# Performance work log

Hardware: AMD Instinct MI355X
Metric: run time of the kernel (lower is better)

Reference implementation:

```python
import jax, jax.numpy as jnp
import numpy as np


def setup_inputs() -> dict:
    key = jax.random.key(0)
    k1, k2, k3, k4, k5 = jax.random.split(key, 5)
    B, N, M, D = 4096, 2048, 2048, 9
    return {
        "x": jax.random.normal(k1, (B, N), dtype=jnp.float32),
        "eternal_weights": jax.random.normal(k2, (D, N, M), dtype=jnp.float32),
        "eternal_biases": jax.random.normal(k3, (M,), dtype=jnp.float32),
        "classical_weights": jax.random.normal(k4, (N, M), dtype=jnp.float32),
        "classical_biases": jax.random.normal(k5, (M,), dtype=jnp.float32),
    }


def _eternal_probs(eternal_weights, n, m):
    # The gate matrix is cos*I - sin*P + sin*P^T with P the circular shift,
    # so (gate @ s)[i] = cos*s[i] - sin*s[(i+1)%n] + sin*s[(i-1)%n].
    # Vectorize over all m output units at once: state is [m, n].
    state0 = jnp.full((m, n), 1.0 / np.sqrt(n), dtype=eternal_weights.dtype)
    angles = eternal_weights[:, :m, :3]  # [D, m, 3] -- weights[depth, j, 0/1/2]

    def gate(state, angle):  # angle: [m]
        c = jnp.cos(angle)[:, None]
        s = jnp.sin(angle)[:, None]
        return c * state - s * jnp.roll(state, -1, axis=1) + s * jnp.roll(state, 1, axis=1)

    def step(state, ang):  # ang: [m, 3] -- consciousness, intelligence, wisdom
        state = gate(state, ang[:, 0])
        state = gate(state, ang[:, 1])
        state = gate(state, ang[:, 2])
        return state, None

    state, _ = jax.lax.scan(step, state0, angles)
    return jnp.abs(state[:, 0]) ** 2  # [m]


def reference(x, eternal_weights, eternal_biases, classical_weights, classical_biases):
    # eternal_biases exists as a parameter in the original module but is unused in forward.
    n = x.shape[1]
    m = classical_weights.shape[1]
    classical = x @ classical_weights + classical_biases  # [B, m]
    probs = _eternal_probs(eternal_weights, n, m)  # [m], identical for every batch row
    return jnp.tanh(classical + probs[None, :])
```

## Files before the change

kernel.cpp:

```cpp
#include <hip/hip_runtime.h>
#include <hip/hip_fp8.h>
#include <stdint.h>

static constexpr int MM = 4096;
static constexpr int KK = 2048;
static constexpr int NN = 2048;

typedef float floatx16 __attribute__((ext_vector_type(16)));
typedef __bf16 bf16x8 __attribute__((ext_vector_type(8)));
typedef unsigned short u16x8 __attribute__((ext_vector_type(8)));
typedef int intx4 __attribute__((ext_vector_type(4)));
typedef int intx8 __attribute__((ext_vector_type(8)));
typedef unsigned char u8x16 __attribute__((ext_vector_type(16)));

__device__ __forceinline__ unsigned short bf16_rne(float x) {
  union { float f; uint32_t u; } c; c.f = x;
  uint32_t u = c.u;
  u += 0x7fffu + ((u >> 16) & 1u);
  return (unsigned short)(u >> 16);
}
__device__ __forceinline__ float bf16_as_f32(unsigned short h) {
  union { float f; uint32_t u; } c; c.u = ((uint32_t)h) << 16;
  return c.f;
}
__device__ __forceinline__ unsigned char f32_to_e4m3(float x) {
  __hip_fp8_e4m3 q(x);
  return (unsigned char)q.__x;
}
__device__ __forceinline__ float fast_tanh(float x) {
  float e = __expf(2.0f * x);
  return 1.0f - 2.0f / (e + 1.0f);
}


__global__ __launch_bounds__(256) void split_x_kernel(
    const float* __restrict__ in, unsigned short* __restrict__ ahi,
    unsigned char* __restrict__ a8, unsigned char* __restrict__ al8,
    int nunits) {
  int idx = blockIdx.x * 256 + threadIdx.x;
  if (idx >= nunits) return;
  int row = idx >> 7;
  int u = idx & 127;
  int g = u >> 2;
  int c4 = u & 3;
  const float4* s = (const float4*)(in + (size_t)row * KK + u * 16);
  float v[16];
#pragma unroll
  for (int q = 0; q < 4; q++) {
    float4 t = s[q];
    v[q * 4 + 0] = t.x; v[q * 4 + 1] = t.y; v[q * 4 + 2] = t.z; v[q * 4 + 3] = t.w;
  }
  unsigned short h[16];
  u8x16 f8, fl8;
#pragma unroll
  for (int e = 0; e < 16; e++) {
    h[e] = bf16_rne(v[e]);
    float lo = v[e] - bf16_as_f32(h[e]);
    f8[e] = f32_to_e4m3(v[e]);
    fl8[e] = f32_to_e4m3(lo * 512.0f);
  }
  size_t rb = (size_t)row * KK;
#pragma unroll
  for (int cc = 0; cc < 2; cc++) {
    int c8 = c4 * 2 + cc;
    int phys8 = (c8 + row + (row >> 3)) & 7;
    u16x8 o;
#pragma unroll
    for (int e = 0; e < 8; e++) o[e] = h[cc * 8 + e];
    *(u16x8*)(ahi + rb + g * 64 + phys8 * 8) = o;
  }
  int phys4 = (c4 + (row >> 1) + (row >> 3)) & 3;
  *(u8x16*)(a8 + rb + g * 64 + phys4 * 16) = f8;
  *(u8x16*)(al8 + rb + g * 64 + phys4 * 16) = fl8;
}

__global__ __launch_bounds__(256) void wsplit_kernel(
    const float* __restrict__ W, unsigned short* __restrict__ bhi,
    unsigned char* __restrict__ b8, unsigned char* __restrict__ bl8) {
  __shared__ float tile[64][65];
  const int tid = threadIdx.x;
  const int n0 = blockIdx.x * 64;
  const int k0 = blockIdx.y * 64;
#pragma unroll
  for (int i = 0; i < 4; i++) {
    int t = tid + i * 256;
    int kr = t >> 4;
    int nc = (t & 15) * 4;
    const float4 v = *(const float4*)(W + (size_t)(k0 + kr) * NN + n0 + nc);
    tile[nc + 0][kr] = v.x;
    tile[nc + 1][kr] = v.y;
    tile[nc + 2][kr] = v.z;
    tile[nc + 3][kr] = v.w;
  }
  __syncthreads();
  const int nl = tid >> 2;
  const int q = tid & 3;
  const int n = n0 + nl;
  float v[16];
  unsigned short h[16];
  u8x16 f8, fl8;
#pragma unroll
  for (int e = 0; e < 16; e++) {
    v[e] = tile[nl][q * 16 + e];
    h[e] = bf16_rne(v[e]);
    float lo = v[e] - bf16_as_f32(h[e]);
    f8[e] = f32_to_e4m3(v[e]);
    fl8[e] = f32_to_e4m3(lo * 512.0f);
  }
  size_t rb = (size_t)n * KK + k0;
#pragma unroll
  for (int cc = 0; cc < 2; cc++) {
    int c8 = q * 2 + cc;
    int phys8 = (c8 + n + (n >> 3)) & 7;
    u16x8 o;
#pragma unroll
    for (int e = 0; e < 8; e++) o[e] = h[cc * 8 + e];
    *(u16x8*)(bhi + rb + phys8 * 8) = o;
  }
  int phys4 = (q + (n >> 1) + (n >> 3)) & 3;
  *(u8x16*)(b8 + rb + phys4 * 16) = f8;
  *(u8x16*)(bl8 + rb + phys4 * 16) = fl8;
}

__global__ __launch_bounds__(64) void bias_probs_kernel(
    const float* __restrict__ E, const float* __restrict__ cb,
    float* __restrict__ bias2) {
  int i = blockIdx.x * 64 + threadIdx.x;
  if (i >= NN) return;
  float p = 1.0f / 2048.0f;
#pragma unroll
  for (int d = 0; d < 9; d++) {
    const float4 a = *(const float4*)(E + (size_t)d * (2048 * 2048) + (size_t)i * 2048);
    float c0 = cosf(a.x), c1 = cosf(a.y), c2 = cosf(a.z);
    p *= (c0 * c0) * (c1 * c1) * (c2 * c2);
  }
  bias2[i] = cb[i] + p;
}

#define GLL(dst, src)                                                        \
  __builtin_amdgcn_global_load_lds(                                          \
      (const __attribute__((address_space(1))) void*)(src),                  \
      (__attribute__((address_space(3))) void*)(dst), 16, 0, 0)

__global__ __launch_bounds__(256, 2) void gemm_tanh_kernel(
    const unsigned short* __restrict__ Ahi, const unsigned char* __restrict__ A8,
    const unsigned char* __restrict__ Al8,
    const unsigned short* __restrict__ Bhi, const unsigned char* __restrict__ B8,
    const unsigned char* __restrict__ Bl8,
    const float* __restrict__ bias2, float* __restrict__ out) {
  __shared__ __align__(16) unsigned short sAh[128 * 64];
  __shared__ __align__(16) unsigned short sBh[128 * 64];
  __shared__ __align__(16) unsigned char sA8[128 * 64];
  __shared__ __align__(16) unsigned char sAl[128 * 64];
  __shared__ __align__(16) unsigned char sB8[128 * 64];
  __shared__ __align__(16) unsigned char sBl[128 * 64];

  const int tid = threadIdx.x;
  const int lane = tid & 63;
  const int wave = tid >> 6;
  const int wm = (wave >> 1) * 64;
  const int wn = (wave & 1) * 64;
  const int bm = blockIdx.y * 128;
  const int bn = blockIdx.x * 128;

  const size_t a16 = (size_t)(bm + (tid >> 3)) * KK + (tid & 7) * 8;
  const size_t b16 = (size_t)(bn + (tid >> 3)) * KK + (tid & 7) * 8;
  const size_t a8b = (size_t)(bm + (tid >> 2)) * KK + (tid & 3) * 16;
  const size_t b8b = (size_t)(bn + (tid >> 2)) * KK + (tid & 3) * 16;
  const int lds16 = tid * 8;
  const int lds8 = tid * 16;

  const int r31 = lane & 31;
  const int half = lane >> 5;

  floatx16 acch[2][2], accc[2][2];
#pragma unroll
  for (int i = 0; i < 2; i++)
#pragma unroll
    for (int j = 0; j < 2; j++)
#pragma unroll
      for (int r = 0; r < 16; r++) { acch[i][j][r] = 0.f; accc[i][j][r] = 0.f; }

  for (int k0 = 0; k0 < KK; k0 += 64) {
#pragma unroll
    for (int p = 0; p < 4; p++) {
      const size_t go = k0 + (size_t)(32 * p) * KK;
      GLL(&sAh[p * 2048 + lds16], Ahi + a16 + go);
      GLL(&sBh[p * 2048 + lds16], Bhi + b16 + go);
    }
#pragma unroll
    for (int p = 0; p < 2; p++) {
      const size_t go = k0 + (size_t)(64 * p) * KK;
      GLL(&sA8[p * 4096 + lds8], A8 + a8b + go);
      GLL(&sAl[p * 4096 + lds8], Al8 + a8b + go);
      GLL(&sB8[p * 4096 + lds8], B8 + b8b + go);
      GLL(&sBl[p * 4096 + lds8], Bl8 + b8b + go);
    }
    __syncthreads();

#pragma unroll
    for (int s = 0; s < 4; s++) {
      const int c8 = s * 2 + half;
      bf16x8 fa[2], fb[2];
#pragma unroll
      for (int t = 0; t < 2; t++) {
        int rowA = wm + t * 32 + r31;
        int ao = rowA * 64 + ((c8 + rowA + (rowA >> 3)) & 7) * 8;
        fa[t] = *(const bf16x8*)(&sAh[ao]);
        int rowB = wn + t * 32 + r31;
        int bo = rowB * 64 + ((c8 + rowB + (rowB >> 3)) & 7) * 8;
        fb[t] = *(const bf16x8*)(&sBh[bo]);
      }
#pragma unroll
      for (int i = 0; i < 2; i++)
#pragma unroll
        for (int j = 0; j < 2; j++)
          acch[i][j] = __builtin_amdgcn_mfma_f32_32x32x16_bf16(fa[i], fb[j], acch[i][j], 0, 0, 0);
    }

    {
      intx8 fal[2], fb8[2];
#pragma unroll
      for (int t = 0; t < 2; t++) {
        int rowA = wm + t * 32 + r31;
        int rowB = wn + t * 32 + r31;
#pragma unroll
        for (int cc = 0; cc < 2; cc++) {
          int c4 = half * 2 + cc;
          int pa = (c4 + (rowA >> 1) + (rowA >> 3)) & 3;
          ((intx4*)&fal[t])[cc] = *(const intx4*)(&sAl[rowA * 64 + pa * 16]);
          int pb = (c4 + (rowB >> 1) + (rowB >> 3)) & 3;
          ((intx4*)&fb8[t])[cc] = *(const intx4*)(&sB8[rowB * 64 + pb * 16]);
        }
      }
#pragma unroll
      for (int i = 0; i < 2; i++)
#pragma unroll
        for (int j = 0; j < 2; j++)
          accc[i][j] = __builtin_amdgcn_mfma_scale_f32_32x32x64_f8f6f4(
              fal[i], fb8[j], accc[i][j], 0, 0, 0, 0x7f7f7f7f, 0, 0x7f7f7f7f);

      intx8 fa8[2], fbl[2];
#pragma unroll
      for (int t = 0; t < 2; t++) {
        int rowA = wm + t * 32 + r31;
        int rowB = wn + t * 32 + r31;
#pragma unroll
        for (int cc = 0; cc < 2; cc++) {
          int c4 = half * 2 + cc;
          int pa = (c4 + (rowA >> 1) + (rowA >> 3)) & 3;
          ((intx4*)&fa8[t])[cc] = *(const intx4*)(&sA8[rowA * 64 + pa * 16]);
          int pb = (c4 + (rowB >> 1) + (rowB >> 3)) & 3;
          ((intx4*)&fbl[t])[cc] = *(const intx4*)(&sBl[rowB * 64 + pb * 16]);
        }
      }
#pragma unroll
      for (int i = 0; i < 2; i++)
#pragma unroll
        for (int j = 0; j < 2; j++)
          accc[i][j] = __builtin_amdgcn_mfma_scale_f32_32x32x64_f8f6f4(
              fa8[i], fbl[j], accc[i][j], 0, 0, 0, 0x7f7f7f7f, 0, 0x7f7f7f7f);
    }
    __syncthreads();
  }

#pragma unroll
  for (int j = 0; j < 2; j++) {
    int col = bn + wn + j * 32 + r31;
    float b2 = bias2[col];
#pragma unroll
    for (int i = 0; i < 2; i++) {
      int row0 = bm + wm + i * 32 + 4 * half;
#pragma unroll
      for (int r = 0; r < 16; r++) {
        int row = row0 + (r & 3) + 8 * (r >> 2);
        float val = acch[i][j][r] + accc[i][j][r] * (1.0f / 512.0f) + b2;
        out[(size_t)row * NN + col] = fast_tanh(val);
      }
    }
  }
}

__global__ __launch_bounds__(256) void fallback_gemm(
    const float* __restrict__ x, const float* __restrict__ E,
    const float* __restrict__ W, const float* __restrict__ cb,
    float* __restrict__ out) {
  __shared__ float sA[16][16];
  __shared__ float sB[16][17];
  __shared__ float sbias[16];
  const int tx = threadIdx.x, ty = threadIdx.y;
  const int row = blockIdx.y * 16 + ty;
  const int col = blockIdx.x * 16 + tx;
  if (ty == 0) {
    float p = 1.0f / 2048.0f;
    for (int d = 0; d < 9; d++) {
      const float* a = E + (size_t)d * (2048 * 2048) + (size_t)col * 2048;
      for (int t = 0; t < 3; t++) { float c = cosf(a[t]); p *= c * c; }
    }
    sbias[tx] = p + cb[col];
  }
  float acc = 0.f;
  for (int k0 = 0; k0 < KK; k0 += 16) {
    __syncthreads();
    sA[ty][tx] = x[(size_t)row * KK + k0 + tx];
    sB[ty][tx] = W[(size_t)(k0 + ty) * NN + col];
    __syncthreads();
#pragma unroll
    for (int kk = 0; kk < 16; kk++) acc += sA[ty][kk] * sB[kk][tx];
  }
  out[(size_t)row * NN + col] = tanhf(acc + sbias[tx]);
}

extern "C" void kernel_launch(void* const* d_in, const int* in_sizes, int n_in,
                              void* d_out, int out_size, void* d_ws, size_t ws_size,
                              hipStream_t stream) {
  const float* x  = (const float*)d_in[0];
  const float* E  = (const float*)d_in[1];
  const float* W  = (const float*)d_in[3];
  const float* cb = (const float*)d_in[4];
  float* out = (float*)d_out;

  const size_t MB = 1024 * 1024;
  const size_t need = 48 * MB + NN * sizeof(float);
  if (ws_size < need) {
    fallback_gemm<<<dim3(NN / 16, MM / 16), dim3(16, 16), 0, stream>>>(x, E, W, cb, out);
    return;
  }

  char* ws = (char*)d_ws;
  unsigned short* Ahi = (unsigned short*)(ws);
  unsigned short* Bhi = (unsigned short*)(ws + 16 * MB);
  unsigned char* A8   = (unsigned char*)(ws + 24 * MB);
  unsigned char* Al8  = (unsigned char*)(ws + 32 * MB);
  unsigned char* B8   = (unsigned char*)(ws + 40 * MB);
  unsigned char* Bl8  = (unsigned char*)(ws + 44 * MB);
  float* bias2 = (float*)(ws + 48 * MB);

  const int nunits = MM * KK / 16;
  split_x_kernel<<<dim3(nunits / 256), dim3(256), 0, stream>>>(x, Ahi, A8, Al8, nunits);
  wsplit_kernel<<<dim3(NN / 64, KK / 64), dim3(256), 0, stream>>>(W, Bhi, B8, Bl8);
  bias_probs_kernel<<<dim3(NN / 64), dim3(64), 0, stream>>>(E, cb, bias2);
  gemm_tanh_kernel<<<dim3(NN / 128, MM / 128), dim3(256), 0, stream>>>(
      Ahi, A8, Al8, Bhi, B8, Bl8, bias2, out);
}
```

Baseline: 311.7 us.

## Merge prepass kernels, group GEMM tile order, and use nontemporal output stores

```diff
diff --git a/kernel.cpp b/kernel.cpp
--- a/kernel.cpp
+++ b/kernel.cpp
@@ -33,108 +33,108 @@
 }
 
 
-__global__ __launch_bounds__(256) void split_x_kernel(
-    const float* __restrict__ in, unsigned short* __restrict__ ahi,
-    unsigned char* __restrict__ a8, unsigned char* __restrict__ al8,
-    int nunits) {
-  int idx = blockIdx.x * 256 + threadIdx.x;
-  if (idx >= nunits) return;
-  int row = idx >> 7;
-  int u = idx & 127;
-  int g = u >> 2;
-  int c4 = u & 3;
-  const float4* s = (const float4*)(in + (size_t)row * KK + u * 16);
-  float v[16];
-#pragma unroll
-  for (int q = 0; q < 4; q++) {
-    float4 t = s[q];
-    v[q * 4 + 0] = t.x; v[q * 4 + 1] = t.y; v[q * 4 + 2] = t.z; v[q * 4 + 3] = t.w;
-  }
-  unsigned short h[16];
-  u8x16 f8, fl8;
-#pragma unroll
-  for (int e = 0; e < 16; e++) {
-    h[e] = bf16_rne(v[e]);
-    float lo = v[e] - bf16_as_f32(h[e]);
-    f8[e] = f32_to_e4m3(v[e]);
-    fl8[e] = f32_to_e4m3(lo * 512.0f);
-  }
-  size_t rb = (size_t)row * KK;
-#pragma unroll
-  for (int cc = 0; cc < 2; cc++) {
-    int c8 = c4 * 2 + cc;
-    int phys8 = (c8 + row + (row >> 3)) & 7;
-    u16x8 o;
-#pragma unroll
-    for (int e = 0; e < 8; e++) o[e] = h[cc * 8 + e];
-    *(u16x8*)(ahi + rb + g * 64 + phys8 * 8) = o;
-  }
-  int phys4 = (c4 + (row >> 1) + (row >> 3)) & 3;
-  *(u8x16*)(a8 + rb + g * 64 + phys4 * 16) = f8;
-  *(u8x16*)(al8 + rb + g * 64 + phys4 * 16) = fl8;
-}
-
-__global__ __launch_bounds__(256) void wsplit_kernel(
-    const float* __restrict__ W, unsigned short* __restrict__ bhi,
-    unsigned char* __restrict__ b8, unsigned char* __restrict__ bl8) {
+__global__ __launch_bounds__(256) void prepass_kernel(
+    const float* __restrict__ x, const float* __restrict__ E,
+    const float* __restrict__ W, const float* __restrict__ cb,
+    unsigned short* __restrict__ ahi, unsigned char* __restrict__ a8,
+    unsigned char* __restrict__ al8,
+    unsigned short* __restrict__ bhi, unsigned char* __restrict__ b8,
+    unsigned char* __restrict__ bl8, float* __restrict__ bias2) {
   __shared__ float tile[64][65];
+  const int blk = blockIdx.x;
   const int tid = threadIdx.x;
-  const int n0 = blockIdx.x * 64;
-  const int k0 = blockIdx.y * 64;
-#pragma unroll
-  for (int i = 0; i < 4; i++) {
-    int t = tid + i * 256;
-    int kr = t >> 4;
-    int nc = (t & 15) * 4;
-    const float4 v = *(const float4*)(W + (size_t)(k0 + kr) * NN + n0 + nc);
-    tile[nc + 0][kr] = v.x;
-    tile[nc + 1][kr] = v.y;
-    tile[nc + 2][kr] = v.z;
-    tile[nc + 3][kr] = v.w;
-  }
-  __syncthreads();
-  const int nl = tid >> 2;
-  const int q = tid & 3;
-  const int n = n0 + nl;
-  float v[16];
-  unsigned short h[16];
-  u8x16 f8, fl8;
-#pragma unroll
-  for (int e = 0; e < 16; e++) {
-    v[e] = tile[nl][q * 16 + e];
-    h[e] = bf16_rne(v[e]);
-    float lo = v[e] - bf16_as_f32(h[e]);
-    f8[e] = f32_to_e4m3(v[e]);
-    fl8[e] = f32_to_e4m3(lo * 512.0f);
-  }
-  size_t rb = (size_t)n * KK + k0;
-#pragma unroll
-  for (int cc = 0; cc < 2; cc++) {
-    int c8 = q * 2 + cc;
-    int phys8 = (c8 + n + (n >> 3)) & 7;
-    u16x8 o;
-#pragma unroll
-    for (int e = 0; e < 8; e++) o[e] = h[cc * 8 + e];
-    *(u16x8*)(bhi + rb + phys8 * 8) = o;
-  }
-  int phys4 = (q + (n >> 1) + (n >> 3)) & 3;
-  *(u8x16*)(b8 + rb + phys4 * 16) = f8;
-  *(u8x16*)(bl8 + rb + phys4 * 16) = fl8;
-}
-
-__global__ __launch_bounds__(64) void bias_probs_kernel(
-    const float* __restrict__ E, const float* __restrict__ cb,
-    float* __restrict__ bias2) {
-  int i = blockIdx.x * 64 + threadIdx.x;
-  if (i >= NN) return;
-  float p = 1.0f / 2048.0f;
-#pragma unroll
-  for (int d = 0; d < 9; d++) {
-    const float4 a = *(const float4*)(E + (size_t)d * (2048 * 2048) + (size_t)i * 2048);
-    float c0 = cosf(a.x), c1 = cosf(a.y), c2 = cosf(a.z);
-    p *= (c0 * c0) * (c1 * c1) * (c2 * c2);
-  }
-  bias2[i] = cb[i] + p;
+
+  if (blk < 2048) {
+    int idx = blk * 256 + tid;
+    int row = idx >> 7;
+    int u = idx & 127;
+    int g = u >> 2;
+    int c4 = u & 3;
+    const float4* s = (const float4*)(x + (size_t)row * KK + u * 16);
+    float v[16];
+#pragma unroll
+    for (int q = 0; q < 4; q++) {
+      float4 t = s[q];
+      v[q * 4 + 0] = t.x; v[q * 4 + 1] = t.y; v[q * 4 + 2] = t.z; v[q * 4 + 3] = t.w;
+    }
+    unsigned short h[16];
+    u8x16 f8, fl8;
+#pragma unroll
+    for (int e = 0; e < 16; e++) {
+      h[e] = bf16_rne(v[e]);
+      float lo = v[e] - bf16_as_f32(h[e]);
+      f8[e] = f32_to_e4m3(v[e]);
+      fl8[e] = f32_to_e4m3(lo * 512.0f);
+    }
+    size_t rb = (size_t)row * KK;
+#pragma unroll
+    for (int cc = 0; cc < 2; cc++) {
+      int c8 = c4 * 2 + cc;
+      int phys8 = (c8 + row + (row >> 3)) & 7;
+      u16x8 o;
+#pragma unroll
+      for (int e = 0; e < 8; e++) o[e] = h[cc * 8 + e];
+      *(u16x8*)(ahi + rb + g * 64 + phys8 * 8) = o;
+    }
+    int phys4 = (c4 + (row >> 1) + (row >> 3)) & 3;
+    *(u8x16*)(a8 + rb + g * 64 + phys4 * 16) = f8;
+    *(u8x16*)(al8 + rb + g * 64 + phys4 * 16) = fl8;
+  } else if (blk < 3072) {
+    const int wb = blk - 2048;
+    const int n0 = (wb & 31) * 64;
+    const int k0 = (wb >> 5) * 64;
+#pragma unroll
+    for (int i = 0; i < 4; i++) {
+      int t = tid + i * 256;
+      int kr = t >> 4;
+      int nc = (t & 15) * 4;
+      const float4 vv = *(const float4*)(W + (size_t)(k0 + kr) * NN + n0 + nc);
+      tile[nc + 0][kr] = vv.x;
+      tile[nc + 1][kr] = vv.y;
+      tile[nc + 2][kr] = vv.z;
+      tile[nc + 3][kr] = vv.w;
+    }
+    __syncthreads();
+    const int nl = tid >> 2;
+    const int q = tid & 3;
+    const int n = n0 + nl;
+    float v[16];
+    unsigned short h[16];
+    u8x16 f8, fl8;
+#pragma unroll
+    for (int e = 0; e < 16; e++) {
+      v[e] = tile[nl][q * 16 + e];
+      h[e] = bf16_rne(v[e]);
+      float lo = v[e] - bf16_as_f32(h[e]);
+      f8[e] = f32_to_e4m3(v[e]);
+      fl8[e] = f32_to_e4m3(lo * 512.0f);
+    }
+    size_t rb = (size_t)n * KK + k0;
+#pragma unroll
+    for (int cc = 0; cc < 2; cc++) {
+      int c8 = q * 2 + cc;
+      int phys8 = (c8 + n + (n >> 3)) & 7;
+      u16x8 o;
+#pragma unroll
+      for (int e = 0; e < 8; e++) o[e] = h[cc * 8 + e];
+      *(u16x8*)(bhi + rb + phys8 * 8) = o;
+    }
+    int phys4 = (q + (n >> 1) + (n >> 3)) & 3;
+    *(u8x16*)(b8 + rb + phys4 * 16) = f8;
+    *(u8x16*)(bl8 + rb + phys4 * 16) = fl8;
+  } else {
+    int i = (blk - 3072) * 256 + tid;
+    if (i < NN) {
+      float p = 1.0f / 2048.0f;
+#pragma unroll
+      for (int d = 0; d < 9; d++) {
+        const float4 a = *(const float4*)(E + (size_t)d * (2048 * 2048) + (size_t)i * 2048);
+        float c0 = cosf(a.x), c1 = cosf(a.y), c2 = cosf(a.z);
+        p *= (c0 * c0) * (c1 * c1) * (c2 * c2);
+      }
+      bias2[i] = cb[i] + p;
+    }
+  }
 }
 
 #define GLL(dst, src)                                                        \
@@ -160,8 +160,11 @@
   const int wave = tid >> 6;
   const int wm = (wave >> 1) * 64;
   const int wn = (wave & 1) * 64;
-  const int bm = blockIdx.y * 128;
-  const int bn = blockIdx.x * 128;
+
+  const int id = blockIdx.x;
+  const int cid = id >> 4, lid = id & 15;
+  const int bm = ((cid >> 2) * 4 + (lid >> 2)) * 128;
+  const int bn = ((cid & 3) * 4 + (lid & 3)) * 128;
 
   const size_t a16 = (size_t)(bm + (tid >> 3)) * KK + (tid & 7) * 8;
   const size_t b16 = (size_t)(bn + (tid >> 3)) * KK + (tid & 7) * 8;
@@ -275,7 +278,7 @@
       for (int r = 0; r < 16; r++) {
         int row = row0 + (r & 3) + 8 * (r >> 2);
         float val = acch[i][j][r] + accc[i][j][r] * (1.0f / 512.0f) + b2;
-        out[(size_t)row * NN + col] = fast_tanh(val);
+        __builtin_nontemporal_store(fast_tanh(val), &out[(size_t)row * NN + col]);
       }
     }
   }
@@ -336,10 +339,8 @@
   unsigned char* Bl8  = (unsigned char*)(ws + 44 * MB);
   float* bias2 = (float*)(ws + 48 * MB);
 
-  const int nunits = MM * KK / 16;
-  split_x_kernel<<<dim3(nunits / 256), dim3(256), 0, stream>>>(x, Ahi, A8, Al8, nunits);
-  wsplit_kernel<<<dim3(NN / 64, KK / 64), dim3(256), 0, stream>>>(W, Bhi, B8, Bl8);
-  bias_probs_kernel<<<dim3(NN / 64), dim3(64), 0, stream>>>(E, cb, bias2);
-  gemm_tanh_kernel<<<dim3(NN / 128, MM / 128), dim3(256), 0, stream>>>(
+  prepass_kernel<<<dim3(3080), dim3(256), 0, stream>>>(
+      x, E, W, cb, Ahi, A8, Al8, Bhi, B8, Bl8, bias2);
+  gemm_tanh_kernel<<<dim3(512), dim3(256), 0, stream>>>(
       Ahi, A8, Al8, Bhi, B8, Bl8, bias2, out);
 }
```

After: 302.9 us. 2.8% less time.
